# Performance work log

Hardware: AMD Instinct MI355X
Metric: run time of the kernel (lower is better)

Reference implementation:

```python
import jax, jax.numpy as jnp
import numpy as np

N = 16000      # points
K = 16         # neighbors per query (fixed-degree CSR)
M = N * K      # attention pairs
C = 384        # embed_dim
H = 6          # num_heads
HD = C // H    # head_dim = 64
L = 25         # quant_grid_length = window/quant = 6.0/0.24
T2 = 2 * L - 1 # rel-pos table length = 49
WIN = 6.0
QUANT = 0.24
SCALE = HD ** -0.5


def setup_inputs() -> dict:
    key = jax.random.key(0)
    ks = jax.random.split(key, 12)
    feats = jax.random.normal(ks[0], (N, C), jnp.float32)
    xyz = jax.random.uniform(ks[1], (N, 3), jnp.float32) * 240.0
    index_0 = jnp.repeat(jnp.arange(N, dtype=jnp.int32), K)            # sorted query ids per pair
    index_0_offsets = jnp.arange(0, M + 1, K, dtype=jnp.int32)         # CSR offsets
    index_1 = jax.random.randint(ks[2], (M,), 0, N, jnp.int32)         # key ids per pair
    sort_idx = jax.random.permutation(ks[3], N).astype(jnp.int32)
    lin = lambda k: jax.random.normal(k, (C, C), jnp.float32) * 0.02
    tab = lambda k: jax.random.normal(k, (T2, 3, H, HD), jnp.float32) * 0.02
    return {
        'feats': feats, 'xyz': xyz,
        'index_0': index_0, 'index_0_offsets': index_0_offsets,
        'index_1': index_1, 'sort_idx': sort_idx,
        'Wq': lin(ks[4]), 'bq': jnp.zeros((C,), jnp.float32),
        'Wk': lin(ks[5]), 'bk': jnp.zeros((C,), jnp.float32),
        'Wv': lin(ks[6]), 'bv': jnp.zeros((C,), jnp.float32),
        'Wp': lin(ks[7]), 'bp': jnp.zeros((C,), jnp.float32),
        'Tq': tab(ks[8]), 'Tk': tab(ks[9]), 'Tv': tab(ks[10]),
    }


def reference(feats, xyz, index_0, index_0_offsets, index_1, sort_idx,
              Wq, bq, Wk, bk, Wv, bv, Wp, bp, Tq, Tk, Tv):
    n = feats.shape[0]
    # QKV projections (key/value default to query feats in the module)
    q = (feats @ Wq.T + bq).reshape(n, H, HD) * SCALE
    k = (feats @ Wk.T + bk).reshape(n, H, HD)
    v = (feats @ Wv.T + bv).reshape(n, H, HD)
    # sort into contiguous-window order
    qs, ks_, vs = q[sort_idx], k[sort_idx], v[sort_idx]
    xyz_s = xyz[sort_idx]
    # quantized in-window coords (shift_win=False -> shift 0)
    xq = jnp.floor(((xyz_s - xyz_s.min(0)) % WIN) / QUANT)             # [N,3], values in [0, L-1]
    i0, i1 = index_0, index_1
    rel_idx = (xq[i0] - xq[i1]).astype(jnp.int32) + (L - 1)            # [M,3] in [0, 2L-2]
    # attention logits: q.k plus contextual relative-position terms
    attn = jnp.einsum('mhd,mhd->mh', qs[i0], ks_[i1])                  # [M,H]
    for t in range(3):
        dq = jnp.einsum('nhd,lhd->nlh', qs, Tq[:, t])                  # [N,T2,H]
        dk = jnp.einsum('nhd,lhd->nlh', ks_, Tk[:, t])
        attn = attn + dq[i0, rel_idx[:, t]] + dk[i1, rel_idx[:, t]]
    # scatter softmax over CSR segments (segments given by index_0)
    amax = jax.ops.segment_max(attn, i0, num_segments=n)
    e = jnp.exp(attn - amax[i0])
    denom = jax.ops.segment_sum(e, i0, num_segments=n)
    a = e / denom[i0]                                                  # [M,H]
    # weighted value aggregation
    x = jax.ops.segment_sum(a[:, :, None] * vs[i1], i0, num_segments=n)  # [N,H,HD]
    # relative-position value contribution, factored through table bins
    for t in range(3):
        seg2 = i0 * T2 + rel_idx[:, t]
        w = jax.ops.segment_sum(a, seg2, num_segments=n * T2).reshape(n, T2, H)
        x = x + jnp.einsum('nlh,lhd->nhd', w, Tv[:, t])
    # unsort back to input order and project
    out = jnp.zeros_like(x).at[sort_idx].set(x).reshape(n, C)
    return out @ Wp.T + bp
```

## Files before the change

kernel.cpp:

```cpp
#include <hip/hip_runtime.h>
#include <hip/hip_bf16.h>
#include <cstdint>
#include <cstddef>

#define NPTS 16000
#define KNB  16
#define CDIM 384
#define NH   6
#define HDIM 64
#define T2C  49
#define NL3T 147
#define THR  160
#define NXC  1152
#define KVROW 256

static constexpr float WIN    = 6.0f;
static constexpr float QUANT  = 0.24f;
static constexpr float QSCALE = 0.125f;
static constexpr float DQS    = 8.0f;
static constexpr float DQSINV = 0.125f;

typedef __attribute__((ext_vector_type(8))) short short8;
typedef __attribute__((ext_vector_type(4))) float floatx4;
typedef __attribute__((ext_vector_type(4))) unsigned short ushort4v;
typedef __attribute__((ext_vector_type(2))) float float2v;

__device__ inline unsigned short f2bf(float x) {
    unsigned int u = __float_as_uint(x);
    unsigned int r = (u + 0x7fffu + ((u >> 16) & 1u)) >> 16;
    return (unsigned short)r;
}
__device__ inline float bf2f(unsigned short b) {
    return __uint_as_float(((unsigned int)b) << 16);
}
__device__ inline float f8tof(unsigned char b) {
    return __builtin_amdgcn_cvt_f32_fp8((int)b, 0);
}
__device__ inline float2v bfpair(unsigned int w) {
    float2v r;
    r.x = __uint_as_float(w << 16);
    r.y = __uint_as_float(w & 0xffff0000u);
    return r;
}

__device__ inline void swz_nh(int& nb, int& h) {
    const int gx   = gridDim.x;
    const int nwg  = gx * NH;
    const int orig = blockIdx.y * gx + blockIdx.x;
    const int q    = nwg >> 3, r = nwg & 7;
    const int xcd  = orig & 7, idx = orig >> 3;
    const int wg   = (xcd < r ? xcd * (q + 1) : r * (q + 1) + (xcd - r) * q) + idx;
    h  = wg / gx;
    nb = wg % gx;
}

__global__ void min_kernel(const float* __restrict__ xyz,
                           unsigned int* __restrict__ minbits) {
    float m0 = INFINITY, m1 = INFINITY, m2 = INFINITY;
    for (int i = blockIdx.x * blockDim.x + threadIdx.x; i < NPTS;
         i += gridDim.x * blockDim.x) {
        m0 = fminf(m0, xyz[i * 3 + 0]);
        m1 = fminf(m1, xyz[i * 3 + 1]);
        m2 = fminf(m2, xyz[i * 3 + 2]);
    }
#pragma unroll
    for (int off = 1; off < 64; off <<= 1) {
        m0 = fminf(m0, __shfl_xor(m0, off, 64));
        m1 = fminf(m1, __shfl_xor(m1, off, 64));
        m2 = fminf(m2, __shfl_xor(m2, off, 64));
    }
    if ((threadIdx.x & 63) == 0) {
        atomicMin(&minbits[0], __float_as_uint(m0));
        atomicMin(&minbits[1], __float_as_uint(m1));
        atomicMin(&minbits[2], __float_as_uint(m2));
    }
}

__global__ void xq_kernel(const float* __restrict__ xyz,
                          const int* __restrict__ sort_idx,
                          const unsigned int* __restrict__ minbits,
                          int* __restrict__ xq) {
    int n = blockIdx.x * blockDim.x + threadIdx.x;
    if (n >= NPTS) return;
    int orig = sort_idx[n];
#pragma unroll
    for (int t = 0; t < 3; ++t) {
        float mn = __uint_as_float(minbits[t]);
        float v  = xyz[orig * 3 + t] - mn;
        float md = fmodf(v, WIN);
        float q  = floorf(md / QUANT);
        xq[n * 3 + t] = (int)q;
    }
}

__global__ void relpack_kernel(const int* __restrict__ idx1,
                               const int* __restrict__ xq,
                               unsigned int* __restrict__ pairs) {
    int m = blockIdx.x * blockDim.x + threadIdx.x;
    if (m >= NPTS * KNB) return;
    int n = m >> 4;
    int key = idx1[m];
    int r0 = xq[n * 3 + 0] - xq[key * 3 + 0] + 24; r0 = min(max(r0, 0), T2C - 1);
    int r1 = xq[n * 3 + 1] - xq[key * 3 + 1] + 24; r1 = min(max(r1, 0), T2C - 1);
    int r2 = xq[n * 3 + 2] - xq[key * 3 + 2] + 24; r2 = min(max(r2, 0), T2C - 1);
    pairs[m] = (unsigned)key | ((unsigned)r0 << 14) | ((unsigned)r1 << 20) |
               ((unsigned)r2 << 26);
}

#define G0 (NPTS * CDIM / 4)
#define G1 (3 * CDIM * CDIM)
#define G2 (CDIM * CDIM)
#define G3 (NH * THR * HDIM)
#define G6 (NH * THR * HDIM)
#define G7 (NH * THR * HDIM)
#define G4 (3 * CDIM)
#define G5 (CDIM)
__global__ void prep_kernel(const float* __restrict__ feats,
                            const int* __restrict__ sortix,
                            const float* __restrict__ Wq,
                            const float* __restrict__ Wk,
                            const float* __restrict__ Wv,
                            const float* __restrict__ Wp,
                            const float* __restrict__ bq,
                            const float* __restrict__ bk,
                            const float* __restrict__ bv,
                            const float* __restrict__ bp,
                            const float* __restrict__ Tv,
                            const float* __restrict__ Tq,
                            const float* __restrict__ Tk,
                            unsigned short* __restrict__ featsbf,
                            unsigned short* __restrict__ Wall,
                            unsigned short* __restrict__ Wpbf,
                            float* __restrict__ Tvh,
                            unsigned short* __restrict__ Tqh,
                            unsigned short* __restrict__ Tkh,
                            float* __restrict__ bfull,
                            float* __restrict__ bproj) {
    int i = blockIdx.x * blockDim.x + threadIdx.x;
    if (i < G0) {
        int n  = i / (CDIM / 4);
        int c4 = (i % (CDIM / 4)) * 4;
        const float4 v = *(const float4*)&feats[(size_t)sortix[n] * CDIM + c4];
        ushort4v o;
        o.x = f2bf(v.x); o.y = f2bf(v.y); o.z = f2bf(v.z); o.w = f2bf(v.w);
        *(ushort4v*)&featsbf[(size_t)n * CDIM + c4] = o;
        return;
    }
    i -= G0;
    if (i < G1) {
        int j = i / CDIM, k = i % CDIM;
        float v = (j < 384) ? Wq[j * CDIM + k]
                : (j < 768) ? Wk[(j - 384) * CDIM + k]
                            : Wv[(j - 768) * CDIM + k];
        Wall[i] = f2bf(v);
        return;
    }
    i -= G1;
    if (i < G2) { Wpbf[i] = f2bf(Wp[i]); return; }
    i -= G2;
    if (i < G3) {
        int jr = (i / HDIM) % THR, d = i % HDIM, h = i / (THR * HDIM);
        Tvh[i] = (jr < NL3T) ? Tv[(size_t)(jr * 6 + h) * HDIM + d] : 0.0f;
        return;
    }
    i -= G3;
    if (i < G6) {
        int jr = (i / HDIM) % THR, d = i % HDIM, h = i / (THR * HDIM);
        Tqh[i] = (jr < NL3T) ? f2bf(Tq[(size_t)(jr * 6 + h) * HDIM + d])
                             : (unsigned short)0;
        return;
    }
    i -= G6;
    if (i < G7) {
        int jr = (i / HDIM) % THR, d = i % HDIM, h = i / (THR * HDIM);
        Tkh[i] = (jr < NL3T) ? f2bf(Tk[(size_t)(jr * 6 + h) * HDIM + d])
                             : (unsigned short)0;
        return;
    }
    i -= G7;
    if (i < G4) {
        bfull[i] = (i < 384) ? bq[i] : (i < 768) ? bk[i - 384] : bv[i - 768];
        return;
    }
    i -= G4;
    if (i < G5) { bproj[i] = bp[i]; }
}

__global__ __launch_bounds__(256) void gemm_big(
    const unsigned short* __restrict__ Abf,
    const unsigned short* __restrict__ Wmat,
    const float* __restrict__ bias,
    int mode,
    unsigned char* __restrict__ qh8, unsigned char* __restrict__ kvh8,
    float* __restrict__ outf) {
    __shared__ unsigned short As[128 * 64];
    __shared__ unsigned short Bs[128 * 64];
    const int tid  = threadIdx.x;
    const int lane = tid & 63;
    const int w    = tid >> 6;
    const int wm   = w >> 1, wn = w & 1;

    const int nwg  = gridDim.x * gridDim.y;
    const int orig = blockIdx.y * gridDim.x + blockIdx.x;
    const int qq   = nwg >> 3, rr = nwg & 7;
    const int xcd  = orig & 7, idx = orig >> 3;
    const int wg   = (xcd < rr ? xcd * (qq + 1) : rr * (qq + 1) + (xcd - rr) * qq) + idx;
    const int jn0  = (wg % gridDim.x) * 128;
    const int m0   = (wg / gridDim.x) * 128;

    floatx4 acc[4][4];
#pragma unroll
    for (int i = 0; i < 4; ++i)
#pragma unroll
        for (int j = 0; j < 4; ++j) acc[i][j] = (floatx4)0.0f;

    for (int kt = 0; kt < 6; ++kt) {
        const int k0 = kt * 64;
#pragma unroll
        for (int q = 0; q < 4; ++q) {
            const int s    = w * 4 + q;
            const int row  = s * 8 + (lane >> 3);
            const int col  = (lane & 7) * 8;
            const unsigned short* ga = Abf  + (size_t)(m0  + row) * CDIM + k0 + col;
            const unsigned short* gb = Wmat + (size_t)(jn0 + row) * CDIM + k0 + col;
            __builtin_amdgcn_global_load_lds(
                (const __attribute__((address_space(1))) void*)ga,
                (__attribute__((address_space(3))) void*)&As[s * 512], 16, 0, 0);
            __builtin_amdgcn_global_load_lds(
                (const __attribute__((address_space(1))) void*)gb,
                (__attribute__((address_space(3))) void*)&Bs[s * 512], 16, 0, 0);
        }
        __syncthreads();
#pragma unroll
        for (int ks = 0; ks < 2; ++ks) {
            short8 a[4], b[4];
#pragma unroll
            for (int mi = 0; mi < 4; ++mi) {
                int row = wm * 64 + mi * 16 + (lane & 15);
                a[mi] = *(const short8*)&As[row * 64 + ks * 32 + (lane >> 4) * 8];
            }
#pragma unroll
            for (int ni = 0; ni < 4; ++ni) {
                int jr = wn * 64 + ni * 16 + (lane & 15);
                b[ni] = *(const short8*)&Bs[jr * 64 + ks * 32 + (lane >> 4) * 8];
            }
#pragma unroll
            for (int mi = 0; mi < 4; ++mi)
#pragma unroll
                for (int ni = 0; ni < 4; ++ni)
                    acc[mi][ni] = __builtin_amdgcn_mfma_f32_16x16x32_bf16(
                        b[ni], a[mi], acc[mi][ni], 0, 0, 0);
        }
        __syncthreads();
    }

#pragma unroll
    for (int mi = 0; mi < 4; ++mi) {
        const int n = m0 + wm * 64 + mi * 16 + (lane & 15);
#pragma unroll
        for (int ni = 0; ni < 4; ++ni) {
            const int jjb = jn0 + wn * 64 + ni * 16 + (lane >> 4) * 4;
            const float4 b4 = *(const float4*)&bias[jjb];
            const float v0 = acc[mi][ni][0] + b4.x;
            const float v1 = acc[mi][ni][1] + b4.y;
            const float v2 = acc[mi][ni][2] + b4.z;
            const float v3 = acc[mi][ni][3] + b4.w;
            if (mode == 0) {
                if (jjb < 384) {
                    const int h = jjb >> 6, d = jjb & 63;
                    ushort4v o;
                    o.x = f2bf(v0 * QSCALE); o.y = f2bf(v1 * QSCALE);
                    o.z = f2bf(v2 * QSCALE); o.w = f2bf(v3 * QSCALE);
                    *(ushort4v*)(qh8 + ((size_t)h * NPTS + n) * 128 + d * 2) = o;
                } else {
                    const int jj = (jjb < 768) ? jjb - 384 : jjb - 768;
                    const int h = jj >> 6, d = jj & 63;
                    const int slot = (jjb < 768) ? 0 : 128;
                    ushort4v o;
                    o.x = f2bf(v0); o.y = f2bf(v1);
                    o.z = f2bf(v2); o.w = f2bf(v3);
                    *(ushort4v*)(kvh8 + ((size_t)h * NPTS + n) * KVROW + slot + d * 2) = o;
                }
            } else {
                float4 o; o.x = v0; o.y = v1; o.z = v2; o.w = v3;
                *(float4*)&outf[(size_t)n * CDIM + jjb] = o;
            }
        }
    }
}

__global__ __launch_bounds__(256) void dqdk_kernel(
    const unsigned char* __restrict__ qh8,
    const unsigned char* __restrict__ kvh8,
    const unsigned short* __restrict__ Tqh,
    const unsigned short* __restrict__ Tkh,
    unsigned char* __restrict__ dqh,
    unsigned char* __restrict__ dkh) {
    __shared__ unsigned short As[128 * 64];
    __shared__ unsigned short Bs[THR * 64];
    const int tid  = threadIdx.x;
    const int lane = tid & 63;
    const int w    = tid >> 6;
    const int wm   = w >> 1, wn = w & 1;
    const int h    = blockIdx.y;
    const bool isk = blockIdx.z != 0;
    const unsigned char* srcb = isk ? kvh8 + (size_t)h * NPTS * KVROW
                                    : qh8  + (size_t)h * NPTS * 128;
    const int sstride = isk ? KVROW : 128;
    unsigned char* dst = (isk ? dkh : dqh) + (size_t)h * NPTS * THR;
    const unsigned short* T = (isk ? Tkh : Tqh) + (size_t)h * THR * HDIM;
    const int m0 = blockIdx.x * 128;

#pragma unroll
    for (int q = 0; q < 4; ++q) {
        const int s   = w * 4 + q;
        const int row = s * 8 + (lane >> 3);
        const unsigned char* ga = srcb + (size_t)(m0 + row) * sstride + (lane & 7) * 16;
        __builtin_amdgcn_global_load_lds(
            (const __attribute__((address_space(1))) void*)ga,
            (__attribute__((address_space(3))) void*)&As[s * 512], 16, 0, 0);
    }
#pragma unroll
    for (int q = 0; q < 5; ++q) {
        const int s   = w * 5 + q;
        const int row = s * 8 + (lane >> 3);
        const unsigned short* gb = T + (size_t)row * HDIM + (lane & 7) * 8;
        __builtin_amdgcn_global_load_lds(
            (const __attribute__((address_space(1))) void*)gb,
            (__attribute__((address_space(3))) void*)&Bs[s * 512], 16, 0, 0);
    }
    __syncthreads();

    floatx4 acc[4][5];
#pragma unroll
    for (int i = 0; i < 4; ++i)
#pragma unroll
        for (int j = 0; j < 5; ++j) acc[i][j] = (floatx4)0.0f;

#pragma unroll
    for (int ks = 0; ks < 2; ++ks) {
        short8 a[4], b[5];
#pragma unroll
        for (int mi = 0; mi < 4; ++mi) {
            int row = wm * 64 + mi * 16 + (lane & 15);
            a[mi] = *(const short8*)&As[row * 64 + ks * 32 + (lane >> 4) * 8];
        }
#pragma unroll
        for (int ni = 0; ni < 5; ++ni) {
            int jr = wn * 80 + ni * 16 + (lane & 15);
            b[ni] = *(const short8*)&Bs[jr * 64 + ks * 32 + (lane >> 4) * 8];
        }
#pragma unroll
        for (int mi = 0; mi < 4; ++mi)
#pragma unroll
            for (int ni = 0; ni < 5; ++ni)
                acc[mi][ni] = __builtin_amdgcn_mfma_f32_16x16x32_bf16(
                    b[ni], a[mi], acc[mi][ni], 0, 0, 0);
    }

#pragma unroll
    for (int mi = 0; mi < 4; ++mi) {
        const int n = m0 + wm * 64 + mi * 16 + (lane & 15);
#pragma unroll
        for (int ni = 0; ni < 5; ++ni) {
            const int jr0 = wn * 80 + ni * 16 + (lane >> 4) * 4;
            int u = __builtin_amdgcn_cvt_pk_fp8_f32(acc[mi][ni][0] * DQS,
                                                    acc[mi][ni][1] * DQS, 0, false);
            u = __builtin_amdgcn_cvt_pk_fp8_f32(acc[mi][ni][2] * DQS,
                                                acc[mi][ni][3] * DQS, u, true);
            *(unsigned int*)(dst + (size_t)n * THR + jr0) = (unsigned)u;
        }
    }
}

__global__ __launch_bounds__(256) void attn_kernel(
    const unsigned char* __restrict__ qh8,
    const unsigned char* __restrict__ kvh8,
    const unsigned int* __restrict__ pairs,
    const unsigned char* __restrict__ dqh,
    const unsigned char* __restrict__ dkh,
    const float* __restrict__ Tvh,
    const int* __restrict__ sortix,
    unsigned short* __restrict__ xb) {
    int nb, h;
    swz_nh(nb, h);
    const int n = nb * 4 + (threadIdx.x >> 6);
    const int lane = threadIdx.x & 63;
    const int pp = lane >> 4, c = lane & 15;
    const int c8 = c * 8;

    const unsigned char* kvb = kvh8 + (size_t)h * NPTS * KVROW;
    const float* Tvb = Tvh + (size_t)h * THR * HDIM;
    const unsigned char* dqn = dqh + ((size_t)h * NPTS + n) * THR;
    const unsigned char* dkb = dkh + (size_t)h * NPTS * THR;

    const uint2 qw = *(const uint2*)(qh8 + ((size_t)h * NPTS + n) * 128 + c8);
    const float2v q01 = bfpair(qw.x), q23 = bfpair(qw.y);

    unsigned int pv[4];
#pragma unroll
    for (int g = 0; g < 4; ++g) pv[g] = pairs[n * KNB + g * 4 + pp];

    int koff[4], t0o[4], t1o[4], t2o[4];
#pragma unroll
    for (int g = 0; g < 4; ++g) {
        koff[g] = (int)(pv[g] & 0x3FFFu) * KVROW + c8;
        t0o[g]  = (int)((pv[g] >> 14) & 63u) * 192 + c * 4;
        t1o[g]  = (int)((pv[g] >> 20) & 63u) * 192 + 64 + c * 4;
        t2o[g]  = (int)(pv[g] >> 26) * 192 + 128 + c * 4;
    }

    float lg[4];
#pragma unroll
    for (int g = 0; g < 4; ++g) {
        const uint2 kw = *(const uint2*)(kvb + koff[g]);
        float2v d = q01 * bfpair(kw.x) + q23 * bfpair(kw.y);
        float part = d.x + d.y;
        if (c < 6) {
            const int t  = (c < 3) ? c : c - 3;
            const int r  = (int)((pv[g] >> (14 + 6 * t)) & 63u);
            const int jr = r * 3 + t;
            const unsigned char* tb =
                (c < 3) ? dqn + jr
                        : dkb + (int)(pv[g] & 0x3FFFu) * THR + jr;
            part += f8tof(*tb) * DQSINV;
        }
        lg[g] = part;
    }
#pragma unroll
    for (int m = 1; m <= 8; m <<= 1)
#pragma unroll
        for (int g = 0; g < 4; ++g) lg[g] += __shfl_xor(lg[g], m, 64);

    float mx = fmaxf(fmaxf(lg[0], lg[1]), fmaxf(lg[2], lg[3]));
    mx = fmaxf(mx, __shfl_xor(mx, 16, 64));
    mx = fmaxf(mx, __shfl_xor(mx, 32, 64));
    float e[4], s = 0.f;
#pragma unroll
    for (int g = 0; g < 4; ++g) { e[g] = __expf(lg[g] - mx); s += e[g]; }
    s += __shfl_xor(s, 16, 64);
    s += __shfl_xor(s, 32, 64);
    const float inv = __builtin_amdgcn_rcpf(s);

    floatx4 xa = (floatx4)0.0f;
#pragma unroll
    for (int g = 0; g < 4; ++g) {
        const float wgt = e[g] * inv;
        const uint2 vw = *(const uint2*)(kvb + koff[g] + 128);
        const float2v v01 = bfpair(vw.x), v23 = bfpair(vw.y);
        floatx4 vv;
        vv[0] = v01.x; vv[1] = v01.y; vv[2] = v23.x; vv[3] = v23.y;
        const floatx4 a0 = *(const floatx4*)&Tvb[t0o[g]];
        const floatx4 a1 = *(const floatx4*)&Tvb[t1o[g]];
        const floatx4 a2 = *(const floatx4*)&Tvb[t2o[g]];
        xa += wgt * (vv + a0 + a1 + a2);
    }
    float xa0 = xa[0], xa1 = xa[1], xa2 = xa[2], xa3 = xa[3];
#pragma unroll
    for (int m = 16; m <= 32; m <<= 1) {
        xa0 += __shfl_xor(xa0, m, 64);
        xa1 += __shfl_xor(xa1, m, 64);
        xa2 += __shfl_xor(xa2, m, 64);
        xa3 += __shfl_xor(xa3, m, 64);
    }
    if (pp == 0) {
        const int dst = sortix[n];
        ushort4v o;
        o.x = f2bf(xa0); o.y = f2bf(xa1); o.z = f2bf(xa2); o.w = f2bf(xa3);
        *(ushort4v*)&xb[(size_t)dst * CDIM + h * HDIM + c * 4] = o;
    }
}

extern "C" void kernel_launch(void* const* d_in, const int* in_sizes, int n_in,
                              void* d_out, int out_size, void* d_ws,
                              size_t ws_size, hipStream_t stream) {
    const float* feats  = (const float*)d_in[0];
    const float* xyz    = (const float*)d_in[1];
    const int*   index1 = (const int*)d_in[4];
    const int*   sortix = (const int*)d_in[5];
    const float* Wq = (const float*)d_in[6];
    const float* bq = (const float*)d_in[7];
    const float* Wk = (const float*)d_in[8];
    const float* bk = (const float*)d_in[9];
    const float* Wv = (const float*)d_in[10];
    const float* bv = (const float*)d_in[11];
    const float* Wp = (const float*)d_in[12];
    const float* bp = (const float*)d_in[13];
    const float* Tq = (const float*)d_in[14];
    const float* Tk = (const float*)d_in[15];
    const float* Tv = (const float*)d_in[16];
    float* out = (float*)d_out;

    char* ws = (char*)d_ws;
    size_t off = 0;
    auto alloc = [&](size_t bytes) -> void* {
        void* p = ws + off;
        off = (off + bytes + 255) & ~(size_t)255;
        return p;
    };
    unsigned short* featsbf = (unsigned short*)alloc((size_t)NPTS * CDIM * 2);
    unsigned short* Wall    = (unsigned short*)alloc((size_t)NXC * CDIM * 2);
    unsigned short* Wpbf    = (unsigned short*)alloc((size_t)CDIM * CDIM * 2);
    float*          Tvh     = (float*)alloc((size_t)NH * THR * HDIM * 4);
    unsigned short* Tqh     = (unsigned short*)alloc((size_t)NH * THR * HDIM * 2);
    unsigned short* Tkh     = (unsigned short*)alloc((size_t)NH * THR * HDIM * 2);
    float*          bfull   = (float*)alloc((size_t)NXC * sizeof(float));
    float*          bproj   = (float*)alloc((size_t)CDIM * sizeof(float));
    unsigned char*  qh8     = (unsigned char*)alloc((size_t)NH * NPTS * 128);
    unsigned char*  kvh8    = (unsigned char*)alloc((size_t)NH * NPTS * KVROW);
    unsigned char*  dqh     = (unsigned char*)alloc((size_t)NH * NPTS * THR);
    unsigned char*  dkh     = (unsigned char*)alloc((size_t)NH * NPTS * THR);
    unsigned int*   pairs   = (unsigned int*)alloc((size_t)NPTS * KNB * 4);
    int*            xq      = (int*)alloc((size_t)NPTS * 3 * sizeof(int));
    unsigned int*   minbits = (unsigned int*)alloc(16);
    unsigned short* xb      = featsbf;

    hipMemsetAsync(minbits, 0x7f, 16, stream);
    min_kernel<<<128, 256, 0, stream>>>(xyz, minbits);
    xq_kernel<<<(NPTS + 255) / 256, 256, 0, stream>>>(xyz, sortix, minbits, xq);
    relpack_kernel<<<(NPTS * KNB + 255) / 256, 256, 0, stream>>>(index1, xq, pairs);

    const int prep_total = G0 + G1 + G2 + G3 + G6 + G7 + G4 + G5;
    prep_kernel<<<(prep_total + 255) / 256, 256, 0, stream>>>(
        feats, sortix, Wq, Wk, Wv, Wp, bq, bk, bv, bp, Tv, Tq, Tk,
        featsbf, Wall, Wpbf, Tvh, Tqh, Tkh, bfull, bproj);

    dim3 g0(NXC / 128, NPTS / 128);
    gemm_big<<<g0, 256, 0, stream>>>(featsbf, Wall, bfull, 0, qh8, kvh8,
                                     (float*)nullptr);

    dim3 gd(NPTS / 128, NH, 2);
    dqdk_kernel<<<gd, 256, 0, stream>>>(qh8, kvh8, Tqh, Tkh, dqh, dkh);

    dim3 ga(NPTS / 4, NH);
    attn_kernel<<<ga, 256, 0, stream>>>(qh8, kvh8, pairs, dqh, dkh, Tvh,
                                        sortix, xb);

    dim3 g1(CDIM / 128, NPTS / 128);
    gemm_big<<<g1, 256, 0, stream>>>(xb, Wpbf, bproj, 1, (unsigned char*)nullptr,
                                     (unsigned char*)nullptr, out);
}
```

Before: 204.0 us.

## Fold key relative-position term into attention dot product, drop dk precompute

Removes the precomputed per-key fp8 dk table and its half of the dqdk GEMM launch. The key-side relative-position term is now computed inline in the attention kernel: each lane loads three bf16 Tk rows for the pair's bins and adds them to q before the dot with k. This trades the dk GEMM pass and its scattered byte gathers for three extra small table loads per pair. The Tk rows are per-head and likely cache-resident, and the term is now evaluated in higher precision than the fp8-stored version.

```diff
diff --git a/kernel.cpp b/kernel.cpp
--- a/kernel.cpp
+++ b/kernel.cpp
@@ -289,13 +289,10 @@
     }
 }
 
-__global__ __launch_bounds__(256) void dqdk_kernel(
+__global__ __launch_bounds__(256) void dq_kernel(
     const unsigned char* __restrict__ qh8,
-    const unsigned char* __restrict__ kvh8,
     const unsigned short* __restrict__ Tqh,
-    const unsigned short* __restrict__ Tkh,
-    unsigned char* __restrict__ dqh,
-    unsigned char* __restrict__ dkh) {
+    unsigned char* __restrict__ dqh) {
     __shared__ unsigned short As[128 * 64];
     __shared__ unsigned short Bs[THR * 64];
     const int tid  = threadIdx.x;
@@ -303,19 +300,16 @@
     const int w    = tid >> 6;
     const int wm   = w >> 1, wn = w & 1;
     const int h    = blockIdx.y;
-    const bool isk = blockIdx.z != 0;
-    const unsigned char* srcb = isk ? kvh8 + (size_t)h * NPTS * KVROW
-                                    : qh8  + (size_t)h * NPTS * 128;
-    const int sstride = isk ? KVROW : 128;
-    unsigned char* dst = (isk ? dkh : dqh) + (size_t)h * NPTS * THR;
-    const unsigned short* T = (isk ? Tkh : Tqh) + (size_t)h * THR * HDIM;
+    const unsigned char* srcb = qh8 + (size_t)h * NPTS * 128;
+    unsigned char* dst = dqh + (size_t)h * NPTS * THR;
+    const unsigned short* T = Tqh + (size_t)h * THR * HDIM;
     const int m0 = blockIdx.x * 128;
 
 #pragma unroll
     for (int q = 0; q < 4; ++q) {
         const int s   = w * 4 + q;
         const int row = s * 8 + (lane >> 3);
-        const unsigned char* ga = srcb + (size_t)(m0 + row) * sstride + (lane & 7) * 16;
+        const unsigned char* ga = srcb + (size_t)(m0 + row) * 128 + (lane & 7) * 16;
         __builtin_amdgcn_global_load_lds(
             (const __attribute__((address_space(1))) void*)ga,
             (__attribute__((address_space(3))) void*)&As[s * 512], 16, 0, 0);
@@ -378,7 +372,7 @@
     const unsigned char* __restrict__ kvh8,
     const unsigned int* __restrict__ pairs,
     const unsigned char* __restrict__ dqh,
-    const unsigned char* __restrict__ dkh,
+    const unsigned short* __restrict__ Tkh,
     const float* __restrict__ Tvh,
     const int* __restrict__ sortix,
     unsigned short* __restrict__ xb) {
@@ -391,8 +385,9 @@
 
     const unsigned char* kvb = kvh8 + (size_t)h * NPTS * KVROW;
     const float* Tvb = Tvh + (size_t)h * THR * HDIM;
+    const unsigned char* tkb =
+        (const unsigned char*)Tkh + (size_t)h * THR * 128;
     const unsigned char* dqn = dqh + ((size_t)h * NPTS + n) * THR;
-    const unsigned char* dkb = dkh + (size_t)h * NPTS * THR;
 
     const uint2 qw = *(const uint2*)(qh8 + ((size_t)h * NPTS + n) * 128 + c8);
     const float2v q01 = bfpair(qw.x), q23 = bfpair(qw.y);
@@ -414,16 +409,17 @@
 #pragma unroll
     for (int g = 0; g < 4; ++g) {
         const uint2 kw = *(const uint2*)(kvb + koff[g]);
-        float2v d = q01 * bfpair(kw.x) + q23 * bfpair(kw.y);
+        const uint2 w0 = *(const uint2*)(tkb + (t0o[g] << 1));
+        const uint2 w1 = *(const uint2*)(tkb + (t1o[g] << 1));
+        const uint2 w2 = *(const uint2*)(tkb + (t2o[g] << 1));
+        const float2v k01 = bfpair(kw.x), k23 = bfpair(kw.y);
+        const float2v ts01 = bfpair(w0.x) + bfpair(w1.x) + bfpair(w2.x);
+        const float2v ts23 = bfpair(w0.y) + bfpair(w1.y) + bfpair(w2.y);
+        float2v d = (q01 + ts01) * k01 + (q23 + ts23) * k23;
         float part = d.x + d.y;
-        if (c < 6) {
-            const int t  = (c < 3) ? c : c - 3;
-            const int r  = (int)((pv[g] >> (14 + 6 * t)) & 63u);
-            const int jr = r * 3 + t;
-            const unsigned char* tb =
-                (c < 3) ? dqn + jr
-                        : dkb + (int)(pv[g] & 0x3FFFu) * THR + jr;
-            part += f8tof(*tb) * DQSINV;
+        if (c < 3) {
+            const int r  = (int)((pv[g] >> (14 + 6 * c)) & 63u);
+            part += f8tof(dqn[r * 3 + c]) * DQSINV;
         }
         lg[g] = part;
     }
@@ -509,7 +505,6 @@
     unsigned char*  qh8     = (unsigned char*)alloc((size_t)NH * NPTS * 128);
     unsigned char*  kvh8    = (unsigned char*)alloc((size_t)NH * NPTS * KVROW);
     unsigned char*  dqh     = (unsigned char*)alloc((size_t)NH * NPTS * THR);
-    unsigned char*  dkh     = (unsigned char*)alloc((size_t)NH * NPTS * THR);
     unsigned int*   pairs   = (unsigned int*)alloc((size_t)NPTS * KNB * 4);
     int*            xq      = (int*)alloc((size_t)NPTS * 3 * sizeof(int));
     unsigned int*   minbits = (unsigned int*)alloc(16);
@@ -529,11 +524,11 @@
     gemm_big<<<g0, 256, 0, stream>>>(featsbf, Wall, bfull, 0, qh8, kvh8,
                                      (float*)nullptr);
 
-    dim3 gd(NPTS / 128, NH, 2);
-    dqdk_kernel<<<gd, 256, 0, stream>>>(qh8, kvh8, Tqh, Tkh, dqh, dkh);
+    dim3 gd(NPTS / 128, NH);
+    dq_kernel<<<gd, 256, 0, stream>>>(qh8, Tqh, dqh);
 
     dim3 ga(NPTS / 4, NH);
-    attn_kernel<<<ga, 256, 0, stream>>>(qh8, kvh8, pairs, dqh, dkh, Tvh,
+    attn_kernel<<<ga, 256, 0, stream>>>(qh8, kvh8, pairs, dqh, Tkh, Tvh,
                                         sortix, xb);
 
     dim3 g1(CDIM / 128, NPTS / 128);
```

Result: slower. 217.4 us (+6.6%).
